# Performance work log

Measured on AMD Instinct MI355X. Metric: run time of the kernel, lower is better.

## Reference

```python
import jax, jax.numpy as jnp
import numpy as np

NEG_SLOPE = 0.2  # PyG GATConv default negative_slope


def gat_conv(x, src, dst, W, a_src, a_dst, b, concat):
    """One PyG-style GATConv (with self-loops already in src/dst).
    x: [N, F_in], W: [F_in, H*C], a_src/a_dst: [H, C], b: [H*C] or [C].
    """
    N = x.shape[0]
    H, C = a_src.shape
    h = (x @ W).reshape(N, H, C)                      # [N,H,C]
    al_s = jnp.einsum('nhc,hc->nh', h, a_src)         # [N,H]
    al_d = jnp.einsum('nhc,hc->nh', h, a_dst)
    e = al_s[src] + al_d[dst]                         # [E,H]
    e = jnp.where(e >= 0, e, NEG_SLOPE * e)           # leaky_relu
    # softmax over edges grouped by destination node
    emax = jax.ops.segment_max(e, dst, num_segments=N)  # [N,H]
    ex = jnp.exp(e - emax[dst])
    denom = jax.ops.segment_sum(ex, dst, num_segments=N)
    alpha = ex / denom[dst]                           # [E,H]
    msg = h[src] * alpha[:, :, None]                  # [E,H,C]
    out = jax.ops.segment_sum(msg, dst, num_segments=N)  # [N,H,C]
    out = out.reshape(N, H * C) if concat else out.mean(axis=1)
    return out + b


def setup_inputs() -> dict:
    key = jax.random.key(0)
    ks = jax.random.split(key, 10)
    N, E = 100000, 1600000
    F_in, Hc, H, F_out = 128, 64, 2, 64
    x = jax.random.normal(ks[0], (N, F_in), dtype=jnp.float32)
    edge_index = jax.random.randint(ks[1], (2, E), 0, N, dtype=jnp.int64)
    s1 = 1.0 / np.sqrt(F_in)
    W1 = jax.random.uniform(ks[2], (F_in, H * Hc), jnp.float32, -s1, s1)
    a_src1 = jax.random.normal(ks[3], (H, Hc), jnp.float32) * 0.1
    a_dst1 = jax.random.normal(ks[4], (H, Hc), jnp.float32) * 0.1
    b1 = jnp.zeros((H * Hc,), jnp.float32)
    s2 = 1.0 / np.sqrt(H * Hc)
    W2 = jax.random.uniform(ks[5], (H * Hc, H * F_out), jnp.float32, -s2, s2)
    a_src2 = jax.random.normal(ks[6], (H, F_out), jnp.float32) * 0.1
    a_dst2 = jax.random.normal(ks[7], (H, F_out), jnp.float32) * 0.1
    b2 = jnp.zeros((F_out,), jnp.float32)
    return {"x": x, "edge_index": edge_index,
            "W1": W1, "a_src1": a_src1, "a_dst1": a_dst1, "b1": b1,
            "W2": W2, "a_src2": a_src2, "a_dst2": a_dst2, "b2": b2}


def reference(x, edge_index, W1, a_src1, a_dst1, b1, W2, a_src2, a_dst2, b2):
    N = x.shape[0]
    loops = jnp.arange(N, dtype=edge_index.dtype)
    src = jnp.concatenate([edge_index[0], loops])  # PyG GATConv adds self-loops
    dst = jnp.concatenate([edge_index[1], loops])
    h = gat_conv(x, src, dst, W1, a_src1, a_dst1, b1, concat=True)
    h = jax.nn.elu(h)
    out = gat_conv(h, src, dst, W2, a_src2, a_dst2, b2, concat=False)
    return out
```

## Files before the change

### kernel.cpp

```cpp
#include <hip/hip_runtime.h>
#include <hip/hip_fp16.h>

#define NEG_SLOPE 0.2f
#define LOG2E 1.4426950408889634f

typedef _Float16 half4v __attribute__((ext_vector_type(4)));
typedef _Float16 half8v __attribute__((ext_vector_type(8)));
typedef float f32x4 __attribute__((ext_vector_type(4)));

__device__ inline unsigned enc_max(float f) {
    unsigned b = __float_as_uint(f);
    return (b & 0x80000000u) ? ~b : (b | 0x80000000u);
}
__device__ inline float dec_max(unsigned k) {
    return (k & 0x80000000u) ? __uint_as_float(k ^ 0x80000000u)
                             : __uint_as_float(~k);
}

__global__ __launch_bounds__(256) void gemm_al_kernel(
    const float* __restrict__ X, const float* __restrict__ W,
    const float* __restrict__ asrc, const float* __restrict__ adst,
    __half* __restrict__ H16, float* __restrict__ AL,
    unsigned* __restrict__ ubp, int N)
{
    __shared__ alignas(16) char smem[49152];

    const int t = threadIdx.x, lane = t & 63, wave = t >> 6;
    const int r0 = blockIdx.x * 64;

#pragma unroll
    for (int i = 0; i < 8; i++) {
        const int f = t + i * 256;
        const int row = f >> 5, k4 = f & 31;
        const int k8 = k4 >> 1, hf = k4 & 1;
        float4 v = make_float4(0.f, 0.f, 0.f, 0.f);
        if (r0 + row < N) v = ((const float4*)X)[(size_t)(r0 + row) * 32 + k4];
        half4v h = { (_Float16)v.x, (_Float16)v.y, (_Float16)v.z, (_Float16)v.w };
        const int slot = row * 16 + (k8 ^ (row & 7));
        *(half4v*)(smem + slot * 16 + hf * 8) = h;
    }
    {
        const int c = t >> 1, kh = t & 1;
        const float* Wc = W + c;
#pragma unroll
        for (int i8 = 0; i8 < 8; i8++) {
            const int k0 = kh * 64 + i8 * 8;
            half8v h;
#pragma unroll
            for (int j = 0; j < 8; j++) h[j] = (_Float16)Wc[(size_t)(k0 + j) * 128];
            const int slot = c * 16 + ((k0 >> 3) ^ (c & 7));
            *(half8v*)(smem + 16384 + slot * 16) = h;
        }
    }
    __syncthreads();

    const int mrow = wave * 16 + (lane & 15);
    const int kg = lane >> 4;
    half4v a[8];
#pragma unroll
    for (int ks = 0; ks < 8; ks++) {
        const int k0 = ks * 16 + kg * 4;
        const int slot = mrow * 16 + ((k0 >> 3) ^ (mrow & 7));
        a[ks] = *(const half4v*)(smem + slot * 16 + (k0 & 7) * 2);
    }
    f32x4 acc[8];
#pragma unroll
    for (int ct = 0; ct < 8; ct++) acc[ct] = (f32x4){0.f, 0.f, 0.f, 0.f};
#pragma unroll
    for (int ct = 0; ct < 8; ct++) {
        const int c = ct * 16 + (lane & 15);
        const char* sbase = smem + 16384 + c * 256;
        const int csw = c & 7;
#pragma unroll
        for (int ks = 0; ks < 8; ks++) {
            const int k0 = ks * 16 + kg * 4;
            const int slot = (k0 >> 3) ^ csw;
            half4v b = *(const half4v*)(sbase + slot * 16 + (k0 & 7) * 2);
            acc[ct] = __builtin_amdgcn_mfma_f32_16x16x16f16(a[ks], b, acc[ct], 0, 0, 0);
        }
    }

    float psh0[4] = {0,0,0,0}, psh1[4] = {0,0,0,0};
    float pdh0[4] = {0,0,0,0}, pdh1[4] = {0,0,0,0};
#pragma unroll
    for (int ct = 0; ct < 8; ct++) {
        const int c = ct * 16 + (lane & 15);
        const float as = asrc[c] * LOG2E, ad = adst[c] * LOG2E;
#pragma unroll
        for (int r = 0; r < 4; r++) {
            if (ct < 4) { psh0[r] = fmaf(acc[ct][r], as, psh0[r]);
                          pdh0[r] = fmaf(acc[ct][r], ad, pdh0[r]); }
            else        { psh1[r] = fmaf(acc[ct][r], as, psh1[r]);
                          pdh1[r] = fmaf(acc[ct][r], ad, pdh1[r]); }
        }
    }
#pragma unroll
    for (int off = 1; off <= 8; off <<= 1) {
#pragma unroll
        for (int r = 0; r < 4; r++) {
            psh0[r] += __shfl_xor(psh0[r], off, 64);
            psh1[r] += __shfl_xor(psh1[r], off, 64);
            pdh0[r] += __shfl_xor(pdh0[r], off, 64);
            pdh1[r] += __shfl_xor(pdh1[r], off, 64);
        }
    }
    float rmax0 = -__builtin_inff(), rmax1 = -__builtin_inff();
    if ((lane & 15) == 0) {
#pragma unroll
        for (int r = 0; r < 4; r++) {
            const int gr = r0 + wave * 16 + (lane >> 4) * 4 + r;
            if (gr < N) {
                ((float4*)AL)[gr] = make_float4(psh0[r], psh1[r], pdh0[r], pdh1[r]);
                rmax0 = fmaxf(rmax0, psh0[r]);
                rmax1 = fmaxf(rmax1, psh1[r]);
            }
        }
    }
#pragma unroll
    for (int off = 32; off > 0; off >>= 1) {
        rmax0 = fmaxf(rmax0, __shfl_xor(rmax0, off, 64));
        rmax1 = fmaxf(rmax1, __shfl_xor(rmax1, off, 64));
    }

    __syncthreads();
    float* Dst = (float*)smem;
    float* red = (float*)(smem + 33792);
    if (lane == 0) { red[wave * 2] = rmax0; red[wave * 2 + 1] = rmax1; }
#pragma unroll
    for (int ct = 0; ct < 8; ct++) {
        const int col = ct * 16 + (lane & 15);
        float* drow = Dst + wave * 2112 + ((lane >> 4) * 4) * 132 + col;
#pragma unroll
        for (int r = 0; r < 4; r++) drow[r * 132] = acc[ct][r];
    }
    __syncthreads();
    if (t < 2) {
        float m = fmaxf(fmaxf(red[t], red[2 + t]), fmaxf(red[4 + t], red[6 + t]));
        atomicMax(&ubp[t], enc_max(m));
    }
#pragma unroll
    for (int i = 0; i < 4; i++) {
        const int f = t + i * 256;
        const int row = f >> 4, c16 = f & 15;
        if (r0 + row < N) {
            const float* src = Dst + (row >> 4) * 2112 + (row & 15) * 132 + c16 * 8;
            const float4 v0 = *(const float4*)src;
            const float4 v1 = *(const float4*)(src + 4);
            half8v h = { (_Float16)v0.x, (_Float16)v0.y, (_Float16)v0.z, (_Float16)v0.w,
                         (_Float16)v1.x, (_Float16)v1.y, (_Float16)v1.z, (_Float16)v1.w };
            *(half8v*)((_Float16*)H16 + (size_t)(r0 + row) * 128 + c16 * 8) = h;
        }
    }
}

__global__ void count_kernel(const int* __restrict__ edst, int* __restrict__ cnt,
                             int E, int N)
{
    int i = blockIdx.x * 256 + threadIdx.x;
    if (i < E)            atomicAdd(&cnt[edst[i]], 1);
    else if (i < E + N)   atomicAdd(&cnt[i - E], 1);
}

__global__ void scan_local_kernel(const int* __restrict__ in, int* __restrict__ out,
                                  int* __restrict__ bsum, int n)
{
    __shared__ int sm[1024];
    const int t = threadIdx.x;
    const int i = blockIdx.x * 1024 + t;
    int v = (i < n) ? in[i] : 0;
    sm[t] = v;
    __syncthreads();
    for (int off = 1; off < 1024; off <<= 1) {
        int x = (t >= off) ? sm[t - off] : 0;
        __syncthreads();
        sm[t] += x;
        __syncthreads();
    }
    if (i < n) out[i] = sm[t];
    if (t == 1023) bsum[blockIdx.x] = sm[t];
}

__global__ void scan_excl_single_kernel(int* __restrict__ a, int B)
{
    __shared__ int sm[1024];
    const int t = threadIdx.x;
    int v = (t < B) ? a[t] : 0;
    sm[t] = v;
    __syncthreads();
    for (int off = 1; off < 1024; off <<= 1) {
        int x = (t >= off) ? sm[t - off] : 0;
        __syncthreads();
        sm[t] += x;
        __syncthreads();
    }
    if (t < B) a[t] = sm[t] - v;
}

__global__ void finalize_csr_kernel(const int* __restrict__ incl,
                                    const int* __restrict__ cnt,
                                    const int* __restrict__ bexcl,
                                    int* __restrict__ dstptr, int* __restrict__ cursor,
                                    int N, int Etot)
{
    const int i = blockIdx.x * 1024 + threadIdx.x;
    if (i < N) {
        int v = incl[i] + bexcl[i >> 10] - cnt[i];
        dstptr[i] = v;
        cursor[i] = v;
    }
    if (i == N) dstptr[N] = Etot;
}

__global__ void scatter_kernel(const int* __restrict__ esrc, const int* __restrict__ edst,
                               int* __restrict__ cursor, int* __restrict__ ssrc,
                               int E, int N, int sliceN, int bps)
{
    const int slice = blockIdx.x & 7;
    const int dlo = slice * sliceN;
    const int dhi = min(N, dlo + sliceN);
    const int Etot = E + N;
    for (int i = (blockIdx.x >> 3) * 256 + (int)threadIdx.x; i < Etot; i += bps * 256) {
        int s, d;
        if (i < E) { s = esrc[i]; d = edst[i]; }
        else       { s = d = i - E; }
        if (d >= dlo && d < dhi) {
            int pos = atomicAdd(&cursor[d], 1);
            ssrc[pos] = s;
        }
    }
}

__global__ __launch_bounds__(128) void aggregate_kernel(
    const __half* __restrict__ H16, const float* __restrict__ AL,
    const int* __restrict__ dstptr, const int* __restrict__ ssrc,
    const unsigned* __restrict__ ubenc, const float* __restrict__ bias,
    float* __restrict__ out, int N, int mode)
{
    const int n = (blockIdx.x * blockDim.x + threadIdx.x) >> 6;
    const int lane = threadIdx.x & 63;
    if (n >= N) return;

    const int beg = dstptr[n], end = dstptr[n + 1];
    const int head = lane >> 5;
    const float ald = AL[(size_t)n * 4 + 2 + head];
    float ub = dec_max(ubenc[head]) + ald;
    ub = fmaxf(ub, NEG_SLOPE * ub);

    const int nblk = (end - beg + 3) >> 2;

    float s = 0.f, a0 = 0.f, a1 = 0.f;

    int   sv0[4], sv1[4], sv2[4];
    float e0[4], e1[4], e2[4];
    unsigned g0[4], g1[4], g2[4];

    auto LSRC = [&](int b, int (&sv)[4]) {
#pragma unroll
        for (int k = 0; k < 4; k++) sv[k] = ssrc[beg + 4 * b + k];
    };
    auto LHE = [&](const int (&sv)[4], float (&e)[4], unsigned (&g)[4]) {
#pragma unroll
        for (int k = 0; k < 4; k++) {
            e[k] = AL[(size_t)sv[k] * 4 + head];
            g[k] = ((const unsigned*)(H16 + (size_t)sv[k] * 128))[lane];
        }
    };
    auto COMP = [&](int t, const float (&e)[4], const unsigned (&g)[4]) {
        const int rem = end - (beg + 4 * t);
#pragma unroll
        for (int k = 0; k < 4; k++) {
            float tt = e[k] + ald;
            tt = fmaxf(tt, NEG_SLOPE * tt);
            float p = exp2f(tt - ub);
            p = (k < rem) ? p : 0.f;
            s += p;
            const float2 f = __half22float2(*(const __half2*)&g[k]);
            a0 = fmaf(p, f.x, a0);
            a1 = fmaf(p, f.y, a1);
        }
    };

    LSRC(0, sv0); LSRC(1, sv1); LSRC(2, sv2);
    LHE(sv0, e0, g0);
    LHE(sv1, e1, g1);

    for (int t = 0; t < nblk; ) {
        LHE(sv2, e2, g2); LSRC(t + 3, sv0); COMP(t, e0, g0); if (++t == nblk) break;
        LHE(sv0, e0, g0); LSRC(t + 3, sv1); COMP(t, e1, g1); if (++t == nblk) break;
        LHE(sv1, e1, g1); LSRC(t + 3, sv2); COMP(t, e2, g2); if (++t == nblk) break;
    }

    const float inv = 1.f / s;
    float o0 = a0 * inv, o1 = a1 * inv;

    if (mode == 0) {
        const float2 b2 = ((const float2*)bias)[lane];
        o0 += b2.x; o1 += b2.y;
        o0 = (o0 > 0.f) ? o0 : (__expf(o0) - 1.f);
        o1 = (o1 > 0.f) ? o1 : (__expf(o1) - 1.f);
        ((float2*)out)[(size_t)n * 64 + lane] = make_float2(o0, o1);
    } else {
        const float q0 = __shfl_xor(o0, 32, 64);
        const float q1 = __shfl_xor(o1, 32, 64);
        if (lane < 32) {
            const float2 b2 = ((const float2*)bias)[lane];
            ((float2*)out)[(size_t)n * 32 + lane] =
                make_float2(0.5f * (o0 + q0) + b2.x, 0.5f * (o1 + q1) + b2.y);
        }
    }
}

extern "C" void kernel_launch(void* const* d_in, const int* in_sizes, int n_in,
                              void* d_out, int out_size, void* d_ws, size_t ws_size,
                              hipStream_t stream)
{
    const float* x   = (const float*)d_in[0];
    const int*   eix = (const int*)d_in[1];
    const float* W1  = (const float*)d_in[2];
    const float* as1 = (const float*)d_in[3];
    const float* ad1 = (const float*)d_in[4];
    const float* b1  = (const float*)d_in[5];
    const float* W2  = (const float*)d_in[6];
    const float* as2 = (const float*)d_in[7];
    const float* ad2 = (const float*)d_in[8];
    const float* b2  = (const float*)d_in[9];
    float* out = (float*)d_out;

    const int N = in_sizes[0] / 128;
    const int E = in_sizes[1] / 2;
    const int Etot = E + N;
    const int* esrc = eix;
    const int* edst = eix + E;

    char* p = (char*)d_ws;
    __half*   h16    = (__half*)p;   p += (size_t)N * 128 * 2;
    float*    y1     = (float*)p;    p += (size_t)N * 128 * 4;
    float*    al     = (float*)p;    p += (size_t)N * 4 * 4;
    int*      cnt    = (int*)p;      p += (size_t)N * 4;
    unsigned* ub     = (unsigned*)p; p += 64;
    int*      incl   = (int*)p;      p += (size_t)N * 4;
    int*      dstptr = (int*)p;      p += (size_t)(N + 1) * 4;
    int*      cursor = (int*)p;      p += (size_t)N * 4;
    int*      bs1    = (int*)p;      p += 1024 * 4;
    int*      ssrc   = (int*)p;      p += (size_t)(Etot + 256) * 4;

    hipMemsetAsync(cnt, 0, (size_t)N * 4 + 64, stream);
    hipMemsetAsync(ssrc + Etot, 0, 256 * 4, stream);

    {
        const int eblocks = (Etot + 255) / 256;
        const int B0 = (N + 1023) / 1024;
        count_kernel<<<eblocks, 256, 0, stream>>>(edst, cnt, E, N);
        scan_local_kernel<<<B0, 1024, 0, stream>>>(cnt, incl, bs1, N);
        scan_excl_single_kernel<<<1, 1024, 0, stream>>>(bs1, B0);
        finalize_csr_kernel<<<(N + 1024) / 1024, 1024, 0, stream>>>(
            incl, cnt, bs1, dstptr, cursor, N, Etot);
        const int sliceN = (N + 7) / 8;
        const int bps = 512;
        scatter_kernel<<<bps * 8, 256, 0, stream>>>(esrc, edst, cursor, ssrc,
                                                    E, N, sliceN, bps);
    }

    const int ggrid = (N + 63) / 64;
    const int ablocks = (N + 1) / 2;

    gemm_al_kernel<<<ggrid, 256, 0, stream>>>(x, W1, as1, ad1, h16, al, ub, N);
    aggregate_kernel<<<ablocks, 128, 0, stream>>>(h16, al, dstptr, ssrc, ub, b1, y1, N, 0);

    gemm_al_kernel<<<ggrid, 256, 0, stream>>>(y1, W2, as2, ad2, h16, al, ub + 2, N);
    aggregate_kernel<<<ablocks, 128, 0, stream>>>(h16, al, dstptr, ssrc, ub + 2, b2, out, N, 1);
}
```

Baseline: 404.7 us.

## Aggregate four destination nodes per wavefront with 16-byte feature loads

The aggregation kernel now assigns 16 lanes per destination node, so each wavefront handles four nodes, and each lane loads a uint4 (8 halfs) of the source feature row instead of 4 bytes. The per-edge index and logit loads are shared by fewer lanes, and there are fewer memory instructions overall. In exchange, the loop trip count becomes the maximum over the four nodes in the wave, which adds idle lanes when degrees differ, and each lane holds more registers for the wider accumulators and prefetch buffers.

```diff
diff --git a/kernel.cpp b/kernel.cpp
--- a/kernel.cpp
+++ b/kernel.cpp
@@ -230,43 +230,53 @@
     }
 }
 
-__global__ __launch_bounds__(128) void aggregate_kernel(
+__global__ __launch_bounds__(256) void aggregate_kernel(
     const __half* __restrict__ H16, const float* __restrict__ AL,
     const int* __restrict__ dstptr, const int* __restrict__ ssrc,
     const unsigned* __restrict__ ubenc, const float* __restrict__ bias,
     float* __restrict__ out, int N, int mode)
 {
-    const int n = (blockIdx.x * blockDim.x + threadIdx.x) >> 6;
+    const int wid  = (blockIdx.x * blockDim.x + threadIdx.x) >> 6;
     const int lane = threadIdx.x & 63;
-    if (n >= N) return;
-
-    const int beg = dstptr[n], end = dstptr[n + 1];
-    const int head = lane >> 5;
-    const float ald = AL[(size_t)n * 4 + 2 + head];
+    if (wid * 4 >= N) return;
+    const int nl   = lane & 15;
+    const int n    = wid * 4 + (lane >> 4);
+    const bool act = (n < N);
+    const int nn   = act ? n : (N - 1);
+    const int beg  = dstptr[nn];
+    const int edges = act ? (dstptr[nn + 1] - beg) : 0;
+
+    const int head = nl >> 3;
+    const float ald = AL[(size_t)nn * 4 + 2 + head];
     float ub = dec_max(ubenc[head]) + ald;
     ub = fmaxf(ub, NEG_SLOPE * ub);
 
-    const int nblk = (end - beg + 3) >> 2;
-
-    float s = 0.f, a0 = 0.f, a1 = 0.f;
+    int tr = (edges + 3) >> 2;
+    tr = max(tr, __shfl_xor(tr, 16, 64));
+    tr = max(tr, __shfl_xor(tr, 32, 64));
+    const int trips = tr;
+
+    float s = 0.f;
+    float a0 = 0.f, a1 = 0.f, a2 = 0.f, a3 = 0.f;
+    float a4 = 0.f, a5 = 0.f, a6 = 0.f, a7 = 0.f;
 
     int   sv0[4], sv1[4], sv2[4];
     float e0[4], e1[4], e2[4];
-    unsigned g0[4], g1[4], g2[4];
+    uint4 g0[4], g1[4], g2[4];
 
     auto LSRC = [&](int b, int (&sv)[4]) {
 #pragma unroll
         for (int k = 0; k < 4; k++) sv[k] = ssrc[beg + 4 * b + k];
     };
-    auto LHE = [&](const int (&sv)[4], float (&e)[4], unsigned (&g)[4]) {
+    auto LHE = [&](const int (&sv)[4], float (&e)[4], uint4 (&g)[4]) {
 #pragma unroll
         for (int k = 0; k < 4; k++) {
             e[k] = AL[(size_t)sv[k] * 4 + head];
-            g[k] = ((const unsigned*)(H16 + (size_t)sv[k] * 128))[lane];
+            g[k] = ((const uint4*)(H16 + (size_t)sv[k] * 128))[nl];
         }
     };
-    auto COMP = [&](int t, const float (&e)[4], const unsigned (&g)[4]) {
-        const int rem = end - (beg + 4 * t);
+    auto COMP = [&](int t, const float (&e)[4], const uint4 (&g)[4]) {
+        const int rem = edges - 4 * t;
 #pragma unroll
         for (int k = 0; k < 4; k++) {
             float tt = e[k] + ald;
@@ -274,9 +284,15 @@
             float p = exp2f(tt - ub);
             p = (k < rem) ? p : 0.f;
             s += p;
-            const float2 f = __half22float2(*(const __half2*)&g[k]);
-            a0 = fmaf(p, f.x, a0);
-            a1 = fmaf(p, f.y, a1);
+            const __half2* ph = (const __half2*)&g[k];
+            const float2 f0 = __half22float2(ph[0]);
+            const float2 f1 = __half22float2(ph[1]);
+            const float2 f2 = __half22float2(ph[2]);
+            const float2 f3 = __half22float2(ph[3]);
+            a0 = fmaf(p, f0.x, a0); a1 = fmaf(p, f0.y, a1);
+            a2 = fmaf(p, f1.x, a2); a3 = fmaf(p, f1.y, a3);
+            a4 = fmaf(p, f2.x, a4); a5 = fmaf(p, f2.y, a5);
+            a6 = fmaf(p, f3.x, a6); a7 = fmaf(p, f3.y, a7);
         }
     };
 
@@ -284,28 +300,50 @@
     LHE(sv0, e0, g0);
     LHE(sv1, e1, g1);
 
-    for (int t = 0; t < nblk; ) {
-        LHE(sv2, e2, g2); LSRC(t + 3, sv0); COMP(t, e0, g0); if (++t == nblk) break;
-        LHE(sv0, e0, g0); LSRC(t + 3, sv1); COMP(t, e1, g1); if (++t == nblk) break;
-        LHE(sv1, e1, g1); LSRC(t + 3, sv2); COMP(t, e2, g2); if (++t == nblk) break;
-    }
-
+    for (int t = 0; t < trips; ) {
+        LHE(sv2, e2, g2); LSRC(t + 3, sv0); COMP(t, e0, g0); if (++t == trips) break;
+        LHE(sv0, e0, g0); LSRC(t + 3, sv1); COMP(t, e1, g1); if (++t == trips) break;
+        LHE(sv1, e1, g1); LSRC(t + 3, sv2); COMP(t, e2, g2); if (++t == trips) break;
+    }
+
+    if (!act) return;
     const float inv = 1.f / s;
-    float o0 = a0 * inv, o1 = a1 * inv;
+    float o0 = a0 * inv, o1 = a1 * inv, o2 = a2 * inv, o3 = a3 * inv;
+    float o4 = a4 * inv, o5 = a5 * inv, o6 = a6 * inv, o7 = a7 * inv;
 
     if (mode == 0) {
-        const float2 b2 = ((const float2*)bias)[lane];
-        o0 += b2.x; o1 += b2.y;
+        const float4 b0 = ((const float4*)bias)[nl * 2];
+        const float4 b1 = ((const float4*)bias)[nl * 2 + 1];
+        o0 += b0.x; o1 += b0.y; o2 += b0.z; o3 += b0.w;
+        o4 += b1.x; o5 += b1.y; o6 += b1.z; o7 += b1.w;
         o0 = (o0 > 0.f) ? o0 : (__expf(o0) - 1.f);
         o1 = (o1 > 0.f) ? o1 : (__expf(o1) - 1.f);
-        ((float2*)out)[(size_t)n * 64 + lane] = make_float2(o0, o1);
+        o2 = (o2 > 0.f) ? o2 : (__expf(o2) - 1.f);
+        o3 = (o3 > 0.f) ? o3 : (__expf(o3) - 1.f);
+        o4 = (o4 > 0.f) ? o4 : (__expf(o4) - 1.f);
+        o5 = (o5 > 0.f) ? o5 : (__expf(o5) - 1.f);
+        o6 = (o6 > 0.f) ? o6 : (__expf(o6) - 1.f);
+        o7 = (o7 > 0.f) ? o7 : (__expf(o7) - 1.f);
+        float4* dst = (float4*)(out + (size_t)n * 128 + nl * 8);
+        dst[0] = make_float4(o0, o1, o2, o3);
+        dst[1] = make_float4(o4, o5, o6, o7);
     } else {
-        const float q0 = __shfl_xor(o0, 32, 64);
-        const float q1 = __shfl_xor(o1, 32, 64);
-        if (lane < 32) {
-            const float2 b2 = ((const float2*)bias)[lane];
-            ((float2*)out)[(size_t)n * 32 + lane] =
-                make_float2(0.5f * (o0 + q0) + b2.x, 0.5f * (o1 + q1) + b2.y);
+        const float q0 = __shfl_xor(o0, 8, 64);
+        const float q1 = __shfl_xor(o1, 8, 64);
+        const float q2 = __shfl_xor(o2, 8, 64);
+        const float q3 = __shfl_xor(o3, 8, 64);
+        const float q4 = __shfl_xor(o4, 8, 64);
+        const float q5 = __shfl_xor(o5, 8, 64);
+        const float q6 = __shfl_xor(o6, 8, 64);
+        const float q7 = __shfl_xor(o7, 8, 64);
+        if (nl < 8) {
+            const float4 b0 = ((const float4*)bias)[nl * 2];
+            const float4 b1 = ((const float4*)bias)[nl * 2 + 1];
+            float4* dst = (float4*)(out + (size_t)n * 64 + nl * 8);
+            dst[0] = make_float4(0.5f * (o0 + q0) + b0.x, 0.5f * (o1 + q1) + b0.y,
+                                 0.5f * (o2 + q2) + b0.z, 0.5f * (o3 + q3) + b0.w);
+            dst[1] = make_float4(0.5f * (o4 + q4) + b1.x, 0.5f * (o5 + q5) + b1.y,
+                                 0.5f * (o6 + q6) + b1.z, 0.5f * (o7 + q7) + b1.w);
         }
     }
 }
@@ -362,11 +400,11 @@
     }
 
     const int ggrid = (N + 63) / 64;
-    const int ablocks = (N + 1) / 2;
+    const int ablocks = (N + 15) / 16;
 
     gemm_al_kernel<<<ggrid, 256, 0, stream>>>(x, W1, as1, ad1, h16, al, ub, N);
-    aggregate_kernel<<<ablocks, 128, 0, stream>>>(h16, al, dstptr, ssrc, ub, b1, y1, N, 0);
+    aggregate_kernel<<<ablocks, 256, 0, stream>>>(h16, al, dstptr, ssrc, ub, b1, y1, N, 0);
 
     gemm_al_kernel<<<ggrid, 256, 0, stream>>>(y1, W2, as2, ad2, h16, al, ub + 2, N);
-    aggregate_kernel<<<ablocks, 128, 0, stream>>>(h16, al, dstptr, ssrc, ub + 2, b2, out, N, 1);
-}
+    aggregate_kernel<<<ablocks, 256, 0, stream>>>(h16, al, dstptr, ssrc, ub + 2, b2, out, N, 1);
+}
```

Result: slower. 418.8 us (+3.5%).
